# Optimization experiments

Hardware: AMD Instinct MI355X
Metric: run time of the kernel (lower is better)

Reference implementation:

```python
import jax, jax.numpy as jnp
import numpy as np

NUM_HEADS = 16
KEY_SIZE = 64
MODEL = NUM_HEADS * KEY_SIZE
B, S = 4, 2048
NEG = jnp.float32(-1e9)


def alibi_bidirectional_bias(num_heads, seq_len):
    # slopes for num_heads//2 heads: 1 / x**(i+1), x = 24**(1/h)
    h = num_heads // 2
    x = 24.0 ** (1.0 / h)
    slopes = (1.0 / x ** jnp.arange(1, h + 1, dtype=jnp.float32))[:, None, None]  # [h,1,1]
    i = jnp.arange(seq_len)
    rel = (i[None, :] - i[:, None]).astype(jnp.float32)  # rel[i,j] = j - i
    # forward (causal): tril(j - i) + (-1e9 strictly above diag)
    fwd = slopes * jnp.tril(rel) + jnp.triu(jnp.full((seq_len, seq_len), NEG), k=1)
    # backward (anti-causal): triu(i - j) + (-1e9 strictly below diag)
    bwd = slopes * jnp.triu(-rel) + jnp.tril(jnp.full((seq_len, seq_len), NEG), k=-1)
    return jnp.concatenate([fwd, bwd], axis=0)  # [num_heads, S, S]


def setup_inputs() -> dict:
    key = jax.random.key(0)
    ks = jax.random.split(key, 11)
    sc = 0.02
    d = {
        "query": jax.random.normal(ks[0], (B, S, MODEL), jnp.float32),
        "key": jax.random.normal(ks[1], (B, S, MODEL), jnp.float32),
        "value": jax.random.normal(ks[2], (B, S, MODEL), jnp.float32),
        "Wq": jax.random.normal(ks[3], (MODEL, MODEL), jnp.float32) * sc,
        "bq": jnp.zeros((MODEL,), jnp.float32),
        "Wk": jax.random.normal(ks[4], (MODEL, MODEL), jnp.float32) * sc,
        "bk": jnp.zeros((MODEL,), jnp.float32),
        "Wv": jax.random.normal(ks[5], (MODEL, MODEL), jnp.float32) * sc,
        "bv": jnp.zeros((MODEL,), jnp.float32),
        "Wo": jax.random.normal(ks[6], (MODEL, MODEL), jnp.float32) * sc,
        "bo": jnp.zeros((MODEL,), jnp.float32),
    }
    return d


def reference(query, key, value, Wq, bq, Wk, bk, Wv, bv, Wo, bo):
    b, s, _ = query.shape
    H, D = NUM_HEADS, KEY_SIZE

    def proj(x, W, bias):
        return (x @ W.T + bias).reshape(b, s, H, D).transpose(0, 2, 1, 3)  # [B,H,S,D]

    q = proj(query, Wq, bq)
    k = proj(key, Wk, bk)
    v = proj(value, Wv, bv)

    bias = alibi_bidirectional_bias(H, s)  # [H,S,S], broadcasts over batch
    scores = jnp.einsum("bhqd,bhkd->bhqk", q, k) / jnp.sqrt(jnp.float32(D)) + bias
    attn = jax.nn.softmax(scores, axis=-1)
    out = jnp.einsum("bhqk,bhkd->bhqd", attn, v)
    out = out.transpose(0, 2, 1, 3).reshape(b, s, H * D)
    return out @ Wo.T + bo
```

## Files before the change

### kernel.cpp

```cpp
#include <hip/hip_runtime.h>
#include <hip/hip_bf16.h>
#include <stdint.h>

typedef unsigned short u16;
typedef __attribute__((ext_vector_type(8))) __bf16 bf16x8;
typedef __attribute__((ext_vector_type(4))) __bf16 bf16x4;
typedef __attribute__((ext_vector_type(4))) float f32x4;

#define S_LEN 2048
#define NHEAD 16
#define HDIM 64
#define DMODEL 1024
#define NBATCH 4
#define MTOK (NBATCH * S_LEN)

__device__ __forceinline__ u16 f2bf(float f) {
    uint32_t u = __float_as_uint(f);
    u += 0x7fffu + ((u >> 16) & 1u);
    return (u16)(u >> 16);
}

__device__ __forceinline__ void gld_lds16(const u16* g, u16* l) {
    __builtin_amdgcn_global_load_lds(
        (const __attribute__((address_space(1))) void*)g,
        (__attribute__((address_space(3))) void*)l, 16, 0, 0);
}

__global__ __launch_bounds__(256) void cast_all(
        const float* __restrict__ q, const float* __restrict__ k, const float* __restrict__ v,
        const float* __restrict__ wq, const float* __restrict__ wk,
        const float* __restrict__ wv, const float* __restrict__ wo,
        u16* __restrict__ xq, u16* __restrict__ xk, u16* __restrict__ xv,
        u16* __restrict__ wqb, u16* __restrict__ wkb, u16* __restrict__ wvb,
        u16* __restrict__ wob) {
    size_t idx4 = (size_t)blockIdx.x * 256 + threadIdx.x;
    const float* src;
    u16* dst;
    size_t off;
    if (idx4 < (size_t)3 << 21) {
        int t = (int)(idx4 >> 21);
        off = (idx4 & ((1u << 21) - 1)) * 4;
        src = (t == 0) ? q : (t == 1) ? k : v;
        dst = (t == 0) ? xq : (t == 1) ? xk : xv;
    } else {
        size_t w = idx4 - ((size_t)3 << 21);
        int t = (int)(w >> 18);
        off = (w & ((1u << 18) - 1)) * 4;
        src = (t == 0) ? wq : (t == 1) ? wk : (t == 2) ? wv : wo;
        dst = (t == 0) ? wqb : (t == 1) ? wkb : (t == 2) ? wvb : wob;
    }
    float4 val = *(const float4*)(src + off);
    ushort4 o;
    o.x = f2bf(val.x); o.y = f2bf(val.y); o.z = f2bf(val.z); o.w = f2bf(val.w);
    *(ushort4*)(dst + off) = o;
}

#define TM 128
#define TN 128
#define BK 64

__device__ __forceinline__ void gemm_body(const u16* __restrict__ A,
                                          const u16* __restrict__ W,
                                          const float* __restrict__ bias,
                                          void* __restrict__ outp, int mode,
                                          int m0, int n0) {
    __shared__ __align__(16) u16 As[2][TM * BK];
    __shared__ __align__(16) u16 Bs[2][TM * BK];
    const int tid  = threadIdx.x;
    const int lane = tid & 63;
    const int wv   = tid >> 6;
    const int l16  = lane & 15;
    const int quad = lane >> 4;
    const int wm   = (wv >> 1) * 64;
    const int wn   = (wv & 1) * 64;

    f32x4 acc[4][4];
#pragma unroll
    for (int i = 0; i < 4; i++)
#pragma unroll
        for (int j = 0; j < 4; j++) acc[i][j] = {};

    const int sr  = lane >> 3;
    const int sc7 = (lane & 7) ^ sr;
    const u16* gA = A + (size_t)(m0 + wv * 32 + sr) * DMODEL + sc7 * 8;
    const u16* gB = W + (size_t)(n0 + wv * 32 + sr) * DMODEL + sc7 * 8;
    const int lofs = wv * 32 * BK;

    const int cA = quad ^ (l16 & 7);
    const int cB = (quad + 4) ^ (l16 & 7);

#pragma unroll
    for (int g = 0; g < 4; g++) {
        gld_lds16(gA + (size_t)(g * 8) * DMODEL, &As[0][lofs + g * 8 * BK]);
        gld_lds16(gB + (size_t)(g * 8) * DMODEL, &Bs[0][lofs + g * 8 * BK]);
    }
    __builtin_amdgcn_s_waitcnt(0x0F70);
    __syncthreads();

    int buf = 0;
    for (int kb = 0; kb < DMODEL; kb += BK) {
        const bool more = (kb + BK < DMODEL);
        if (more) {
#pragma unroll
            for (int g = 0; g < 4; g++) {
                gld_lds16(gA + kb + BK + (size_t)(g * 8) * DMODEL,
                          &As[buf ^ 1][lofs + g * 8 * BK]);
                gld_lds16(gB + kb + BK + (size_t)(g * 8) * DMODEL,
                          &Bs[buf ^ 1][lofs + g * 8 * BK]);
            }
        }
        __builtin_amdgcn_sched_barrier(0);

        bf16x8 af0[4], af1[4], bf0[4], bf1[4];
#pragma unroll
        for (int i = 0; i < 4; i++) {
            const u16* ap = &As[buf][(wm + i * 16 + l16) * BK];
            af0[i] = *(const bf16x8*)(ap + cA * 8);
            af1[i] = *(const bf16x8*)(ap + cB * 8);
        }
#pragma unroll
        for (int j = 0; j < 4; j++) {
            const u16* bp = &Bs[buf][(wn + j * 16 + l16) * BK];
            bf0[j] = *(const bf16x8*)(bp + cA * 8);
            bf1[j] = *(const bf16x8*)(bp + cB * 8);
        }
#pragma unroll
        for (int i = 0; i < 4; i++)
#pragma unroll
            for (int j = 0; j < 4; j++)
                acc[i][j] = __builtin_amdgcn_mfma_f32_16x16x32_bf16(af0[i], bf0[j], acc[i][j], 0, 0, 0);
#pragma unroll
        for (int i = 0; i < 4; i++)
#pragma unroll
            for (int j = 0; j < 4; j++)
                acc[i][j] = __builtin_amdgcn_mfma_f32_16x16x32_bf16(af1[i], bf1[j], acc[i][j], 0, 0, 0);

        if (more) __builtin_amdgcn_s_waitcnt(0x0F70);
        __syncthreads();
        buf ^= 1;
    }

#pragma unroll
    for (int j = 0; j < 4; j++) {
        int n = n0 + wn + j * 16 + l16;
        float bv = bias[n];
#pragma unroll
        for (int i = 0; i < 4; i++) {
            int mbase = m0 + wm + i * 16 + quad * 4;
#pragma unroll
            for (int r = 0; r < 4; r++) {
                int m = mbase + r;
                float v = acc[i][j][r] + bv;
                if (mode == 2) {
                    ((float*)outp)[(size_t)m * DMODEL + n] = v;
                } else {
                    int b = m >> 11, s = m & (S_LEN - 1);
                    int h = n >> 6, d = n & 63;
                    u16* o = (u16*)outp;
                    size_t idx = (mode == 0)
                        ? ((((size_t)(b * NHEAD + h)) * S_LEN + s) * HDIM + d)
                        : ((((size_t)(b * NHEAD + h)) * HDIM + d) * S_LEN + s);
                    o[idx] = f2bf(v);
                }
            }
        }
    }
}

__device__ __forceinline__ void gemm_coords(int& m0, int& n0) {
    const int lid = blockIdx.x + 8 * blockIdx.y;
    const int xcd = lid & 7;
    const int s   = lid >> 3;
    n0 = (s & 7) * TN;
    m0 = ((s >> 3) + 8 * xcd) * TM;
}

__global__ __launch_bounds__(256) void gemm_qkv(
        const u16* __restrict__ xq, const u16* __restrict__ xk, const u16* __restrict__ xv,
        const u16* __restrict__ wq, const u16* __restrict__ wk, const u16* __restrict__ wv,
        const float* __restrict__ bq, const float* __restrict__ bk, const float* __restrict__ bv,
        u16* __restrict__ Qb, u16* __restrict__ Kb, u16* __restrict__ Vb) {
    int z = blockIdx.z;
    const u16* A   = (z == 0) ? xq : (z == 1) ? xk : xv;
    const u16* W   = (z == 0) ? wq : (z == 1) ? wk : wv;
    const float* b = (z == 0) ? bq : (z == 1) ? bk : bv;
    u16* out       = (z == 0) ? Qb : (z == 1) ? Kb : Vb;
    int m0, n0;
    gemm_coords(m0, n0);
    gemm_body(A, W, b, out, (z == 2) ? 1 : 0, m0, n0);
}

__global__ __launch_bounds__(256) void gemm_one(
        const u16* __restrict__ A, const u16* __restrict__ W,
        const float* __restrict__ bias, void* __restrict__ out, int mode) {
    int m0, n0;
    gemm_coords(m0, n0);
    gemm_body(A, W, bias, out, mode, m0, n0);
}

__global__ __launch_bounds__(256, 4) void flash_kernel(
        const u16* __restrict__ Q, const u16* __restrict__ K,
        const u16* __restrict__ Vt, u16* __restrict__ AO) {
    __shared__ __align__(16) u16 Ksm[2][64 * 64];
    __shared__ __align__(16) u16 Vsm[2][64 * 64];
    __shared__ __align__(16) u16 Psm[4][16 * 64];

    const int tid  = threadIdx.x;
    const int wv   = tid >> 6;
    const int lane = tid & 63;
    const int l16  = lane & 15;
    const int quad = lane >> 4;

    const int lid   = blockIdx.x + 16 * blockIdx.y;
    const int xcd   = lid & 7;
    const int slot  = lid >> 3;
    const int bh    = xcd + 8 * (slot >> 4);
    const int g_idx = slot & 15;

    const int h    = bh & (NHEAD - 1);
    const int b    = bh >> 4;
    const bool fwd = (h < 8);
    const int sgn  = fwd ? 1 : -1;
    const float slope2 = __builtin_amdgcn_exp2f(-(float)((h & 7) + 1) * 0.5731203125901445f)
                         * 1.4426950408889634f;
    const float cL = 0.18033688011112042f;

    const u16* Kg = K + (size_t)bh * S_LEN * HDIM;
    const u16* Vg = Vt + (size_t)bh * HDIM * S_LEN;

    const int sr = lane >> 3;
    const int sc = (lane & 7) ^ sr;
    const int r0 = 16 * wv;

    const int cA = quad ^ (l16 & 7);
    const int cB = (quad + 4) ^ (l16 & 7);

    float brt[4][4];
#pragma unroll
    for (int t = 0; t < 4; t++)
#pragma unroll
        for (int r = 0; r < 4; r++)
            brt[t][r] = slope2 * (float)(sgn * (16 * t + 4 * quad + r - l16)) - 16.0f;

    int poff4[4];
#pragma unroll
    for (int t = 0; t < 4; t++)
        poff4[t] = l16 * 64 + (((2 * t + (quad >> 1)) ^ (l16 & 7)) * 8) + 4 * (quad & 1);

    bf16x8 ones;
#pragma unroll
    for (int j = 0; j < 8; j++) ones[j] = (__bf16)1.0f;

    const float dkq = slope2 * (float)(sgn * 64);

#pragma unroll 1
    for (int half = 0; half < 2; half++) {
        const int g  = half ? (31 - g_idx) : g_idx;
        const int q0 = g * 64 + wv * 16;
        const u16* Qp = Q + ((size_t)bh * S_LEN + q0) * HDIM;
        const bf16x8 aq0 = *(const bf16x8*)(Qp + l16 * HDIM + quad * 8);
        const bf16x8 aq1 = *(const bf16x8*)(Qp + l16 * HDIM + 32 + quad * 8);

        f32x4 o[4], osum = {};
#pragma unroll
        for (int dt = 0; dt < 4; dt++) o[dt] = {};

        const int kt0 = fwd ? 0 : g;
        const int kt1 = fwd ? g : (S_LEN / 64 - 1);

        __syncthreads();
        const u16* kg = Kg + ((size_t)(kt0 * 64) + r0 + sr) * 64 + sc * 8;
        const u16* vg = Vg + (size_t)(r0 + sr) * S_LEN + kt0 * 64 + sc * 8;
        gld_lds16(kg,              &Ksm[0][r0 * 64]);
        gld_lds16(kg + 8 * 64,     &Ksm[0][(r0 + 8) * 64]);
        gld_lds16(vg,              &Vsm[0][r0 * 64]);
        gld_lds16(vg + 8 * S_LEN,  &Vsm[0][(r0 + 8) * 64]);
        kg += 64 * 64;
        vg += 64;

        float kq = slope2 * (float)(sgn * (kt0 * 64 - q0));

        int buf = 0;
        for (int kt = kt0; kt <= kt1; ++kt) {
            __builtin_amdgcn_s_waitcnt(0x0F70);
            __syncthreads();
            if (kt < kt1) {
                gld_lds16(kg,             &Ksm[buf ^ 1][r0 * 64]);
                gld_lds16(kg + 8 * 64,    &Ksm[buf ^ 1][(r0 + 8) * 64]);
                gld_lds16(vg,             &Vsm[buf ^ 1][r0 * 64]);
                gld_lds16(vg + 8 * S_LEN, &Vsm[buf ^ 1][(r0 + 8) * 64]);
                kg += 64 * 64;
                vg += 64;
            }
            const u16* Ks = &Ksm[buf][0];
            const u16* Vs = &Vsm[buf][0];

            f32x4 st[4];
            __builtin_amdgcn_s_setprio(1);
#pragma unroll
            for (int t = 0; t < 4; t++) {
                const u16* kp = Ks + (16 * t + l16) * 64;
                bf16x8 k0 = *(const bf16x8*)(kp + cA * 8);
                bf16x8 k1 = *(const bf16x8*)(kp + cB * 8);
                f32x4 c = {};
                c = __builtin_amdgcn_mfma_f32_16x16x32_bf16(k0, aq0, c, 0, 0, 0);
                c = __builtin_amdgcn_mfma_f32_16x16x32_bf16(k1, aq1, c, 0, 0, 0);
                st[t] = c;
            }
            __builtin_amdgcn_s_setprio(0);

            float p[4][4];
            if (kt == g) {
                const int qg = q0 + l16;
#pragma unroll
                for (int t = 0; t < 4; t++)
#pragma unroll
                    for (int r = 0; r < 4; r++) {
                        const int kg2 = kt * 64 + 16 * t + 4 * quad + r;
                        const bool ok = fwd ? (kg2 <= qg) : (kg2 >= qg);
                        float s2 = fmaf(st[t][r], cL, brt[t][r] + kq);
                        p[t][r] = ok ? __builtin_amdgcn_exp2f(s2) : 0.0f;
                    }
            } else {
#pragma unroll
                for (int t = 0; t < 4; t++)
#pragma unroll
                    for (int r = 0; r < 4; r++)
                        p[t][r] = __builtin_amdgcn_exp2f(fmaf(st[t][r], cL, brt[t][r] + kq));
            }
            kq += dkq;

            u16* Pw = &Psm[wv][0];
#pragma unroll
            for (int t = 0; t < 4; t++) {
                bf16x4 pk;
                pk[0] = (__bf16)p[t][0];
                pk[1] = (__bf16)p[t][1];
                pk[2] = (__bf16)p[t][2];
                pk[3] = (__bf16)p[t][3];
                *(bf16x4*)(Pw + poff4[t]) = pk;
            }
            __builtin_amdgcn_s_waitcnt(0xC07F);
            bf16x8 pf0 = *(const bf16x8*)(&Pw[l16 * 64 + cA * 8]);
            bf16x8 pf1 = *(const bf16x8*)(&Pw[l16 * 64 + cB * 8]);

            __builtin_amdgcn_s_setprio(1);
#pragma unroll
            for (int dt = 0; dt < 4; dt++) {
                const u16* vp = Vs + (dt * 16 + l16) * 64;
                bf16x8 v0 = *(const bf16x8*)(vp + cA * 8);
                bf16x8 v1 = *(const bf16x8*)(vp + cB * 8);
                o[dt] = __builtin_amdgcn_mfma_f32_16x16x32_bf16(pf0, v0, o[dt], 0, 0, 0);
                o[dt] = __builtin_amdgcn_mfma_f32_16x16x32_bf16(pf1, v1, o[dt], 0, 0, 0);
            }
            osum = __builtin_amdgcn_mfma_f32_16x16x32_bf16(pf0, ones, osum, 0, 0, 0);
            osum = __builtin_amdgcn_mfma_f32_16x16x32_bf16(pf1, ones, osum, 0, 0, 0);
            __builtin_amdgcn_s_setprio(0);
            buf ^= 1;
        }

#pragma unroll
        for (int r = 0; r < 4; r++) {
            float inv = 1.0f / osum[r];
            int qg = q0 + quad * 4 + r;
            u16* op = AO + ((size_t)b * S_LEN + qg) * DMODEL + h * HDIM;
#pragma unroll
            for (int dt = 0; dt < 4; dt++)
                op[dt * 16 + l16] = f2bf(o[dt][r] * inv);
        }
    }
}

extern "C" void kernel_launch(void* const* d_in, const int* in_sizes, int n_in,
                              void* d_out, int out_size, void* d_ws, size_t ws_size,
                              hipStream_t stream) {
    const float* query = (const float*)d_in[0];
    const float* key   = (const float*)d_in[1];
    const float* value = (const float*)d_in[2];
    const float* Wq    = (const float*)d_in[3];
    const float* bq    = (const float*)d_in[4];
    const float* Wk    = (const float*)d_in[5];
    const float* bk    = (const float*)d_in[6];
    const float* Wv    = (const float*)d_in[7];
    const float* bv    = (const float*)d_in[8];
    const float* Wo    = (const float*)d_in[9];
    const float* bo    = (const float*)d_in[10];

    const size_t Xe = (size_t)MTOK * DMODEL;
    const size_t We = (size_t)DMODEL * DMODEL;
    u16* xq  = (u16*)d_ws;
    u16* xk  = xq + Xe;
    u16* xv  = xk + Xe;
    u16* wqb = xv + Xe;
    u16* wkb = wqb + We;
    u16* wvb = wkb + We;
    u16* wob = wvb + We;
    u16* Qb  = wob + We;
    u16* Kb  = Qb + Xe;
    u16* Vb  = Kb + Xe;
    u16* AO  = xq;

    cast_all<<<dim3(28672), dim3(256), 0, stream>>>(
        query, key, value, Wq, Wk, Wv, Wo,
        xq, xk, xv, wqb, wkb, wvb, wob);

    gemm_qkv<<<dim3(DMODEL / TN, MTOK / TM, 3), dim3(256), 0, stream>>>(
        xq, xk, xv, wqb, wkb, wvb, bq, bk, bv, Qb, Kb, Vb);

    flash_kernel<<<dim3(16, NBATCH * NHEAD), dim3(256), 0, stream>>>(Qb, Kb, Vb, AO);

    gemm_one<<<dim3(DMODEL / TN, MTOK / TM, 1), dim3(256), 0, stream>>>(AO, wob, bo, d_out, 2);
}
```

Baseline: 309.1 us.

## Use 8-wave GEMM blocks with triple-buffered LDS pipeline

Rewrites the projection GEMM body to use 512 threads (8 waves, each computing a 64x32 sub-tile) and a three-stage LDS ring buffer with two tiles prefetched ahead, using vmcnt-based partial waits and raw s_barrier. The goal is to hide global-to-LDS load latency better and raise wave occupancy per CU during the GEMMs. In exchange LDS use per block grows by half and each wave gets less MFMA reuse per LDS read, which could lower occupancy or raise LDS traffic.

```diff
diff --git a/kernel.cpp b/kernel.cpp
--- a/kernel.cpp
+++ b/kernel.cpp
@@ -58,90 +58,99 @@
 #define TM 128
 #define TN 128
 #define BK 64
+#define KT (DMODEL / BK)
 
 __device__ __forceinline__ void gemm_body(const u16* __restrict__ A,
                                           const u16* __restrict__ W,
                                           const float* __restrict__ bias,
                                           void* __restrict__ outp, int mode,
                                           int m0, int n0) {
-    __shared__ __align__(16) u16 As[2][TM * BK];
-    __shared__ __align__(16) u16 Bs[2][TM * BK];
+    __shared__ __align__(16) u16 As[3][TM * BK];
+    __shared__ __align__(16) u16 Bs[3][TN * BK];
     const int tid  = threadIdx.x;
     const int lane = tid & 63;
     const int wv   = tid >> 6;
     const int l16  = lane & 15;
     const int quad = lane >> 4;
-    const int wm   = (wv >> 1) * 64;
-    const int wn   = (wv & 1) * 64;
-
-    f32x4 acc[4][4];
+    const int wm   = (wv >> 2) * 64;
+    const int wn   = (wv & 3) * 32;
+
+    f32x4 acc[4][2];
 #pragma unroll
     for (int i = 0; i < 4; i++)
 #pragma unroll
-        for (int j = 0; j < 4; j++) acc[i][j] = {};
+        for (int j = 0; j < 2; j++) acc[i][j] = {};
 
     const int sr  = lane >> 3;
     const int sc7 = (lane & 7) ^ sr;
-    const u16* gA = A + (size_t)(m0 + wv * 32 + sr) * DMODEL + sc7 * 8;
-    const u16* gB = W + (size_t)(n0 + wv * 32 + sr) * DMODEL + sc7 * 8;
-    const int lofs = wv * 32 * BK;
+    const u16* gA = A + (size_t)(m0 + wv * 16 + sr) * DMODEL + sc7 * 8;
+    const u16* gB = W + (size_t)(n0 + wv * 16 + sr) * DMODEL + sc7 * 8;
+    const int lofs = wv * 16 * BK;
 
     const int cA = quad ^ (l16 & 7);
     const int cB = (quad + 4) ^ (l16 & 7);
 
-#pragma unroll
-    for (int g = 0; g < 4; g++) {
-        gld_lds16(gA + (size_t)(g * 8) * DMODEL, &As[0][lofs + g * 8 * BK]);
-        gld_lds16(gB + (size_t)(g * 8) * DMODEL, &Bs[0][lofs + g * 8 * BK]);
-    }
-    __builtin_amdgcn_s_waitcnt(0x0F70);
-    __syncthreads();
-
-    int buf = 0;
-    for (int kb = 0; kb < DMODEL; kb += BK) {
-        const bool more = (kb + BK < DMODEL);
-        if (more) {
-#pragma unroll
-            for (int g = 0; g < 4; g++) {
-                gld_lds16(gA + kb + BK + (size_t)(g * 8) * DMODEL,
-                          &As[buf ^ 1][lofs + g * 8 * BK]);
-                gld_lds16(gB + kb + BK + (size_t)(g * 8) * DMODEL,
-                          &Bs[buf ^ 1][lofs + g * 8 * BK]);
-            }
+#define STG(b, t) do { \
+    gld_lds16(gA + (size_t)(t) * BK,                    &As[b][lofs]); \
+    gld_lds16(gA + (size_t)(t) * BK + 8 * DMODEL,       &As[b][lofs + 8 * BK]); \
+    gld_lds16(gB + (size_t)(t) * BK,                    &Bs[b][lofs]); \
+    gld_lds16(gB + (size_t)(t) * BK + 8 * DMODEL,       &Bs[b][lofs + 8 * BK]); \
+} while (0)
+
+    STG(0, 0);
+    STG(1, 1);
+    __builtin_amdgcn_s_waitcnt(0x0F74);
+    __builtin_amdgcn_sched_barrier(0);
+    __builtin_amdgcn_s_barrier();
+    __builtin_amdgcn_sched_barrier(0);
+
+    int bc = 0;
+#pragma unroll 1
+    for (int t = 0; t < KT; ++t) {
+        if (t + 2 < KT) {
+            int bs = bc + 2; if (bs >= 3) bs -= 3;
+            STG(bs, t + 2);
         }
         __builtin_amdgcn_sched_barrier(0);
 
-        bf16x8 af0[4], af1[4], bf0[4], bf1[4];
+        bf16x8 af0[4], af1[4], bf0[2], bf1[2];
 #pragma unroll
         for (int i = 0; i < 4; i++) {
-            const u16* ap = &As[buf][(wm + i * 16 + l16) * BK];
+            const u16* ap = &As[bc][(wm + i * 16 + l16) * BK];
             af0[i] = *(const bf16x8*)(ap + cA * 8);
             af1[i] = *(const bf16x8*)(ap + cB * 8);
         }
 #pragma unroll
-        for (int j = 0; j < 4; j++) {
-            const u16* bp = &Bs[buf][(wn + j * 16 + l16) * BK];
+        for (int j = 0; j < 2; j++) {
+            const u16* bp = &Bs[bc][(wn + j * 16 + l16) * BK];
             bf0[j] = *(const bf16x8*)(bp + cA * 8);
             bf1[j] = *(const bf16x8*)(bp + cB * 8);
         }
 #pragma unroll
         for (int i = 0; i < 4; i++)
 #pragma unroll
-            for (int j = 0; j < 4; j++)
+            for (int j = 0; j < 2; j++)
                 acc[i][j] = __builtin_amdgcn_mfma_f32_16x16x32_bf16(af0[i], bf0[j], acc[i][j], 0, 0, 0);
 #pragma unroll
         for (int i = 0; i < 4; i++)
 #pragma unroll
-            for (int j = 0; j < 4; j++)
+            for (int j = 0; j < 2; j++)
                 acc[i][j] = __builtin_amdgcn_mfma_f32_16x16x32_bf16(af1[i], bf1[j], acc[i][j], 0, 0, 0);
 
-        if (more) __builtin_amdgcn_s_waitcnt(0x0F70);
-        __syncthreads();
-        buf ^= 1;
+        if (t + 2 < KT) {
+            __builtin_amdgcn_s_waitcnt(0x0F74);
+        } else if (t + 1 < KT) {
+            __builtin_amdgcn_s_waitcnt(0x0F70);
+        }
+        __builtin_amdgcn_sched_barrier(0);
+        __builtin_amdgcn_s_barrier();
+        __builtin_amdgcn_sched_barrier(0);
+        if (++bc == 3) bc = 0;
     }
-
-#pragma unroll
-    for (int j = 0; j < 4; j++) {
+#undef STG
+
+#pragma unroll
+    for (int j = 0; j < 2; j++) {
         int n = n0 + wn + j * 16 + l16;
         float bv = bias[n];
 #pragma unroll
@@ -175,7 +184,7 @@
     m0 = ((s >> 3) + 8 * xcd) * TM;
 }
 
-__global__ __launch_bounds__(256) void gemm_qkv(
+__global__ __launch_bounds__(512, 2) void gemm_qkv(
         const u16* __restrict__ xq, const u16* __restrict__ xk, const u16* __restrict__ xv,
         const u16* __restrict__ wq, const u16* __restrict__ wk, const u16* __restrict__ wv,
         const float* __restrict__ bq, const float* __restrict__ bk, const float* __restrict__ bv,
@@ -190,7 +199,7 @@
     gemm_body(A, W, b, out, (z == 2) ? 1 : 0, m0, n0);
 }
 
-__global__ __launch_bounds__(256) void gemm_one(
+__global__ __launch_bounds__(512, 2) void gemm_one(
         const u16* __restrict__ A, const u16* __restrict__ W,
         const float* __restrict__ bias, void* __restrict__ out, int mode) {
     int m0, n0;
@@ -404,10 +413,10 @@
         query, key, value, Wq, Wk, Wv, Wo,
         xq, xk, xv, wqb, wkb, wvb, wob);
 
-    gemm_qkv<<<dim3(DMODEL / TN, MTOK / TM, 3), dim3(256), 0, stream>>>(
+    gemm_qkv<<<dim3(DMODEL / TN, MTOK / TM, 3), dim3(512), 0, stream>>>(
         xq, xk, xv, wqb, wkb, wvb, bq, bk, bv, Qb, Kb, Vb);
 
     flash_kernel<<<dim3(16, NBATCH * NHEAD), dim3(256), 0, stream>>>(Qb, Kb, Vb, AO);
 
-    gemm_one<<<dim3(DMODEL / TN, MTOK / TM, 1), dim3(256), 0, stream>>>(AO, wob, bo, d_out, 2);
-}
+    gemm_one<<<dim3(DMODEL / TN, MTOK / TM), dim3(512), 0, stream>>>(AO, wob, bo, d_out, 2);
+}
```

New measurement: 363.0 us. 17.5% more time.
